# Optimization experiments

Measured on AMD Instinct MI355X. Metric: run time of the kernel, lower is better.

Reference implementation:

```python
import jax, jax.numpy as jnp
import numpy as np

EPS = 1e-5
TOPK = 4

def bn(x, gamma, beta, mean, var, axis=1):
    # inference-mode batchnorm (running stats)
    shp = [1] * x.ndim
    shp[axis] = -1
    scale = (gamma / jnp.sqrt(var + EPS)).reshape(shp)
    shift = (beta - mean * gamma / jnp.sqrt(var + EPS)).reshape(shp)
    return x * scale + shift


def setup_inputs() -> dict:
    key = jax.random.key(0)
    ks = jax.random.split(key, 4)
    B, C, T, H, W = 8, 512, 8, 28, 28
    R = 64
    Cq = C // 4
    s = 0.05
    return {
        "input": jax.random.normal(ks[0], (B, C, T, H, W), dtype=jnp.float32),
        "w_reduce": jax.random.normal(ks[1], (R, C), dtype=jnp.float32) * s,
        "bn1_gamma": jnp.ones((R,), jnp.float32), "bn1_beta": jnp.zeros((R,), jnp.float32),
        "bn1_mean": jnp.zeros((R,), jnp.float32), "bn1_var": jnp.ones((R,), jnp.float32),
        "w_proj": jax.random.normal(ks[2], (Cq, C + 2), dtype=jnp.float32) * s,
        "bn2_gamma": jnp.ones((Cq,), jnp.float32), "bn2_beta": jnp.zeros((Cq,), jnp.float32),
        "bn2_mean": jnp.zeros((Cq,), jnp.float32), "bn2_var": jnp.ones((Cq,), jnp.float32),
        "w_t": jax.random.normal(ks[3], (C, Cq, 3, 1), dtype=jnp.float32) * s,
        "bn3_gamma": jnp.ones((C,), jnp.float32), "bn3_beta": jnp.zeros((C,), jnp.float32),
        "bn3_mean": jnp.zeros((C,), jnp.float32), "bn3_var": jnp.ones((C,), jnp.float32),
    }


def reference(input, w_reduce, bn1_gamma, bn1_beta, bn1_mean, bn1_var,
              w_proj, bn2_gamma, bn2_beta, bn2_mean, bn2_var,
              w_t, bn3_gamma, bn3_beta, bn3_mean, bn3_var):
    x = input
    B, C, T, H, W = x.shape
    R = w_reduce.shape[0]
    K = TOPK
    HW = H * W

    # spatial template from frame 0
    template_d = x[:, :, 0].reshape(B, C, HW)                                  # (B,C,HW)
    template_p = bn(jnp.einsum('rc,bcs->brs', w_reduce, template_d),
                    bn1_gamma, bn1_beta, bn1_mean, bn1_var)                     # (B,R,HW)
    spt_inds = jnp.argmax(template_p, axis=2)                                  # (B,R)
    template_resample = jnp.take_along_axis(template_d, spt_inds[:, None, :], axis=2)  # (B,C,R)

    x_flat = x.reshape(B, C, T * HW)
    affinity = jnp.einsum('bcr,bcs->brs', template_resample, x_flat)           # (B,R,T*HW)
    affinity = affinity.reshape(B, R, T, HW)
    _, topk_inds = jax.lax.top_k(affinity, K)                                  # (B,R,T,K)
    inds = jnp.transpose(topk_inds, (0, 3, 2, 1))                              # (B,K,T,R)

    # gather trajectory features: traj[b,k,c,t,r] = x[b,c,t, inds[b,k,t,r]]
    x4 = x.reshape(B, C, T, HW)
    traj = jnp.take_along_axis(x4[:, None], inds[:, :, None], axis=4)          # (B,K,C,T,R)
    traj_bk = traj.reshape(B * K, C, T, R)

    inds_bk = inds.reshape(B * K, 1, T, R)
    row = (inds_bk // W).astype(jnp.float32) / H
    col = (inds_bk % W).astype(jnp.float32) / W
    coords = jnp.concatenate([row, col], axis=1)                               # (B*K,2,T,R)

    fuse = jnp.concatenate([traj_bk, coords], axis=1)                          # (B*K,C+2,T,R)
    fuse = bn(jnp.einsum('qc,bctr->bqtr', w_proj, fuse),
              bn2_gamma, bn2_beta, bn2_mean, bn2_var)                          # (B*K,C/4,T,R)
    fuse = fuse.reshape(B, K, C // 4, T, R).max(axis=1)                        # (B,C/4,T,R)

    tc = jax.lax.conv_general_dilated(fuse, w_t, window_strides=(1, 1),
                                      padding=((1, 1), (0, 0)),
                                      dimension_numbers=('NCHW', 'OIHW', 'NCHW'))
    tc = jax.nn.relu(bn(tc, bn3_gamma, bn3_beta, bn3_mean, bn3_var))           # (B,C,T,R)

    points = traj.mean(axis=1).reshape(B, C, T * R)                            # (B,C,T*R)
    proj = jnp.einsum('bcp,bcs->bps', points, x_flat)                          # (B,T*R,T*HW)
    proj = jax.nn.softmax(proj, axis=1)                                        # softmax over T*R (dim=1)
    prop = jnp.einsum('bcp,bps->bcs', tc.reshape(B, C, T * R), proj)           # (B,C,T*HW)
    return x + prop.reshape(B, C, T, H, W)
```

## Files before the change

kernel.cpp:

```cpp
#include <hip/hip_runtime.h>

#define EPSB 1e-5f

#define B_   8
#define C_   512
#define T_   8
#define HW_  784
#define S_   6272
#define R_   64
#define CQ_  128
#define K_   4
#define P_   512

typedef _Float16 f16;
typedef __attribute__((ext_vector_type(8))) _Float16 f16x8;
typedef __attribute__((ext_vector_type(4))) _Float16 f16x4;
typedef __attribute__((ext_vector_type(4))) float    f32x4;

#define OB_PTST  0ull
#define OB_TC    4194304ull
#define OB_D     8388608ull
#define OB_TRH   8589312ull
#define OB_TRF   9113600ull
#define OB_INDS  10162176ull
#define OB_WRH   10227712ull
#define OB_WPH   10293248ull
#define OB_WTH   10424320ull
#define OB_XT    10817536ull
#define T_TPA    62197760ull
#define T_AFF    63803392ull
#define T_FUSEK  62197760ull
#define T_FUSE   66392064ull
#define CHB      62197760ull

__device__ __forceinline__ void gload16(const void* g, void* l) {
    __builtin_amdgcn_global_load_lds(
        (const __attribute__((address_space(1))) unsigned int*)g,
        (__attribute__((address_space(3))) unsigned int*)l, 16, 0, 0);
}

__global__ __launch_bounds__(256) void k_prep(
    const float* __restrict__ wr, const float* __restrict__ wp,
    const float* __restrict__ wt,
    f16* __restrict__ wrh, f16* __restrict__ wph, f16* __restrict__ wth)
{
    int i = blockIdx.x*256 + threadIdx.x;
    if (i < 32768) {
        wrh[i] = (f16)wr[i];
    } else if (i < 98304) {
        int j = i - 32768;
        int q = j >> 9, c = j & 511;
        wph[j] = (f16)wp[q*514 + c];
    } else {
        int j = i - 98304;
        int co = j / 384;
        int rem = j - co*384;
        int dt = rem >> 7, ci = rem & 127;
        wth[j] = (f16)wt[(size_t)(co*CQ_ + ci)*3 + dt];
    }
}

__global__ __launch_bounds__(256) void k_xpose(
    const float* __restrict__ x, f16* __restrict__ xT)
{
    __shared__ float tile[64][65];
    int s0 = blockIdx.x*64, c0 = blockIdx.y*64, b = blockIdx.z;
    int tid = threadIdx.x;
    #pragma unroll
    for (int i = 0; i < 4; ++i) {
        int idx = tid + i*256;
        int cl = idx >> 4, s4 = (idx & 15)*4;
        f32x4 v = *(const f32x4*)&x[((size_t)(b*C_ + c0+cl))*S_ + s0 + s4];
        tile[cl][s4] = v.x; tile[cl][s4+1] = v.y;
        tile[cl][s4+2] = v.z; tile[cl][s4+3] = v.w;
    }
    __syncthreads();
    #pragma unroll
    for (int i = 0; i < 4; ++i) {
        int idx = tid + i*256;
        int sl = idx >> 4, c4 = (idx & 15)*4;
        f16x4 h;
        h[0] = (f16)tile[c4+0][sl]; h[1] = (f16)tile[c4+1][sl];
        h[2] = (f16)tile[c4+2][sl]; h[3] = (f16)tile[c4+3][sl];
        *(f16x4*)&xT[((size_t)(b*S_ + s0+sl))*C_ + c0 + c4] = h;
    }
}

__global__ __launch_bounds__(256) void k_templ(
    const f16* __restrict__ xT, const f16* __restrict__ wrh,
    float* __restrict__ tpa)
{
    __shared__ __align__(16) f16 As[128*64];
    __shared__ __align__(16) f16 Bs[64*64];
    int b = blockIdx.y; int s0 = blockIdx.x*128;
    int tid = threadIdx.x;
    int lane = tid & 63, w = tid >> 6;
    int lrow = lane >> 3;
    int swzc = ((lane & 7) ^ lrow) * 8;
    const f16* ga = xT  + ((size_t)b*S_ + s0 + w*32 + lrow)*C_ + swzc;
    const f16* gb = wrh + (size_t)(w*16 + lrow)*C_ + swzc;
    int mbase = (w & 1)*64, nbase = (w >> 1)*32;
    int fr = lane & 15, quad = lane >> 4;
    int sw = fr & 7;
    f32x4 acc[4][2] = {};
    for (int c0 = 0; c0 < C_; c0 += 64) {
        #pragma unroll
        for (int j = 0; j < 4; ++j)
            gload16(ga + j*8*C_, &As[(w*32 + j*8)*64]);
        #pragma unroll
        for (int j = 0; j < 2; ++j)
            gload16(gb + j*8*C_, &Bs[(w*16 + j*8)*64]);
        ga += 64; gb += 64;
        __syncthreads();
        #pragma unroll
        for (int kk = 0; kk < 2; ++kk) {
            int ch = ((kk*4 + quad) ^ sw) * 8;
            f16x8 af[4], bf[2];
            #pragma unroll
            for (int mt = 0; mt < 4; ++mt)
                af[mt] = *(const f16x8*)&As[(mbase + mt*16 + fr)*64 + ch];
            #pragma unroll
            for (int nt = 0; nt < 2; ++nt)
                bf[nt] = *(const f16x8*)&Bs[(nbase + nt*16 + fr)*64 + ch];
            #pragma unroll
            for (int mt = 0; mt < 4; ++mt)
                #pragma unroll
                for (int nt = 0; nt < 2; ++nt)
                    acc[mt][nt] = __builtin_amdgcn_mfma_f32_16x16x32_f16(
                        af[mt], bf[nt], acc[mt][nt], 0, 0, 0);
        }
        __syncthreads();
    }
    #pragma unroll
    for (int mt = 0; mt < 4; ++mt) {
        int sb = s0 + mbase + mt*16 + quad*4;
        if (sb < HW_) {
            #pragma unroll
            for (int nt = 0; nt < 2; ++nt) {
                int r = nbase + nt*16 + fr;
                *(f32x4*)&tpa[((size_t)(b*R_ + r))*HW_ + sb] = acc[mt][nt];
            }
        }
    }
}

__global__ __launch_bounds__(256) void k_targmax(
    const float* __restrict__ x, const float* __restrict__ wr_g,
    const float* __restrict__ g1, const float* __restrict__ v1,
    const float* __restrict__ tpa,
    float* __restrict__ trf, f16* __restrict__ trh)
{
    __shared__ float row[HW_];
    __shared__ float sval[256];
    __shared__ int   sidx[256];
    __shared__ float cval[4];
    __shared__ int   cidx[4];
    __shared__ float eval_[4];
    __shared__ int   bestind;
    int bid = blockIdx.x;
    int b = bid >> 6, r = bid & 63;
    int tid = threadIdx.x;
    float sc = g1[r] * rsqrtf(v1[r] + EPSB);
    const float* tprow = tpa + (size_t)bid*HW_;
    for (int s = tid; s < HW_; s += 256) row[s] = tprow[s]*sc;
    __syncthreads();
    for (int pass = 0; pass < 4; ++pass) {
        float best = -INFINITY; int bi = 0;
        for (int s = tid; s < HW_; s += 256) {
            float v = row[s];
            if (v > best) { best = v; bi = s; }
        }
        sval[tid] = best; sidx[tid] = bi;
        __syncthreads();
        for (int off = 128; off > 0; off >>= 1) {
            if (tid < off) {
                float ov = sval[tid+off]; int oi = sidx[tid+off];
                if (ov > sval[tid] || (ov == sval[tid] && oi < sidx[tid])) {
                    sval[tid] = ov; sidx[tid] = oi;
                }
            }
            __syncthreads();
        }
        if (tid == 0) {
            cval[pass] = sval[0]; cidx[pass] = sidx[0];
            row[sidx[0]] = -INFINITY;
        }
        __syncthreads();
    }
    float thr = 0.05f * fabsf(sc);
    if (cval[0] - cval[1] >= thr) {
        if (tid == 0) bestind = cidx[0];
    } else {
        int w = tid >> 6, lane = tid & 63;
        int cand = cidx[w];
        float sum = 0.f;
        #pragma unroll
        for (int i = 0; i < 8; ++i) {
            int c = lane + i*64;
            sum += wr_g[r*C_ + c] * x[((size_t)(b*C_ + c))*S_ + cand];
        }
        #pragma unroll
        for (int off = 32; off > 0; off >>= 1) sum += __shfl_xor(sum, off);
        if (lane == 0) eval_[w] = sum*sc;
        __syncthreads();
        if (tid == 0) {
            float bv = eval_[0]; int bi2 = cidx[0];
            for (int j = 1; j < 4; ++j) {
                float v = eval_[j]; int ii = cidx[j];
                if (v > bv || (v == bv && ii < bi2)) { bv = v; bi2 = ii; }
            }
            bestind = bi2;
        }
    }
    __syncthreads();
    int ind = bestind;
    for (int c = tid; c < C_; c += 256) {
        float v = x[((size_t)(b*C_ + c))*S_ + ind];
        trf[(size_t)bid*C_ + c] = v;
        trh[(size_t)bid*C_ + c] = (f16)v;
    }
}

__global__ __launch_bounds__(256) void k_affin(
    const f16* __restrict__ xT, const f16* __restrict__ trh,
    float* __restrict__ aff)
{
    __shared__ __align__(16) f16 As[128*64];
    __shared__ __align__(16) f16 Bs[64*64];
    int b = blockIdx.y; int s0 = blockIdx.x*128;
    int tid = threadIdx.x;
    int lane = tid & 63, w = tid >> 6;
    int lrow = lane >> 3;
    int swzc = ((lane & 7) ^ lrow) * 8;
    const f16* ga = xT  + ((size_t)b*S_ + s0 + w*32 + lrow)*C_ + swzc;
    const f16* gb = trh + ((size_t)(b*R_) + w*16 + lrow)*C_ + swzc;
    int mbase = (w & 1)*64, nbase = (w >> 1)*32;
    int fr = lane & 15, quad = lane >> 4;
    int sw = fr & 7;
    f32x4 acc[4][2] = {};
    for (int c0 = 0; c0 < C_; c0 += 64) {
        #pragma unroll
        for (int j = 0; j < 4; ++j)
            gload16(ga + j*8*C_, &As[(w*32 + j*8)*64]);
        #pragma unroll
        for (int j = 0; j < 2; ++j)
            gload16(gb + j*8*C_, &Bs[(w*16 + j*8)*64]);
        ga += 64; gb += 64;
        __syncthreads();
        #pragma unroll
        for (int kk = 0; kk < 2; ++kk) {
            int ch = ((kk*4 + quad) ^ sw) * 8;
            f16x8 af[4], bf[2];
            #pragma unroll
            for (int mt = 0; mt < 4; ++mt)
                af[mt] = *(const f16x8*)&As[(mbase + mt*16 + fr)*64 + ch];
            #pragma unroll
            for (int nt = 0; nt < 2; ++nt)
                bf[nt] = *(const f16x8*)&Bs[(nbase + nt*16 + fr)*64 + ch];
            #pragma unroll
            for (int mt = 0; mt < 4; ++mt)
                #pragma unroll
                for (int nt = 0; nt < 2; ++nt)
                    acc[mt][nt] = __builtin_amdgcn_mfma_f32_16x16x32_f16(
                        af[mt], bf[nt], acc[mt][nt], 0, 0, 0);
        }
        __syncthreads();
    }
    #pragma unroll
    for (int mt = 0; mt < 4; ++mt) {
        int sb = s0 + mbase + mt*16 + quad*4;
        #pragma unroll
        for (int nt = 0; nt < 2; ++nt) {
            int r = nbase + nt*16 + fr;
            *(f32x4*)&aff[((size_t)(b*R_ + r))*S_ + sb] = acc[mt][nt];
        }
    }
}

__global__ __launch_bounds__(256) void k_topk(
    const float* __restrict__ x, const float* __restrict__ trf,
    const float* __restrict__ aff, int* __restrict__ inds)
{
    __shared__ float row[HW_];
    __shared__ float sval[256];
    __shared__ int   sidx[256];
    __shared__ float cval[8];
    __shared__ int   cidx[8];
    __shared__ float eval_[8];
    int r = blockIdx.x, t = blockIdx.y, b = blockIdx.z;
    int tid = threadIdx.x;
    const float* arow = aff + ((size_t)(b*R_ + r))*S_ + t*HW_;
    for (int s = tid; s < HW_; s += 256) row[s] = arow[s];
    __syncthreads();
    for (int pass = 0; pass < 8; ++pass) {
        float best = -INFINITY; int bi = 0;
        for (int s = tid; s < HW_; s += 256) {
            float v = row[s];
            if (v > best) { best = v; bi = s; }
        }
        sval[tid] = best; sidx[tid] = bi;
        __syncthreads();
        for (int off = 128; off > 0; off >>= 1) {
            if (tid < off) {
                float ov = sval[tid+off]; int oi = sidx[tid+off];
                if (ov > sval[tid] || (ov == sval[tid] && oi < sidx[tid])) {
                    sval[tid] = ov; sidx[tid] = oi;
                }
            }
            __syncthreads();
        }
        if (tid == 0) {
            cval[pass] = sval[0]; cidx[pass] = sidx[0];
            row[sidx[0]] = -INFINITY;
        }
        __syncthreads();
    }
    if (cval[3] - cval[4] >= 0.35f) {
        if (tid < K_)
            inds[((b*K_ + tid)*T_ + t)*R_ + r] = cidx[tid];
    } else {
        int w = tid >> 6, lane = tid & 63;
        #pragma unroll
        for (int half = 0; half < 2; ++half) {
            int j = w + half*4;
            int cand = cidx[j];
            float sum = 0.f;
            #pragma unroll
            for (int i = 0; i < 8; ++i) {
                int c = lane + i*64;
                sum += trf[((size_t)(b*R_ + r))*C_ + c]
                     * x[((size_t)(b*C_ + c))*S_ + t*HW_ + cand];
            }
            #pragma unroll
            for (int off = 32; off > 0; off >>= 1) sum += __shfl_xor(sum, off);
            if (lane == 0) eval_[j] = sum;
        }
        __syncthreads();
        if (tid == 0) {
            unsigned used = 0;
            for (int k = 0; k < K_; ++k) {
                float bv = -INFINITY; int bj = -1;
                for (int j = 0; j < 8; ++j) {
                    if (used & (1u << j)) continue;
                    float v = eval_[j]; int ii = cidx[j];
                    if (bj < 0 || v > bv || (v == bv && ii < cidx[bj])) {
                        bv = v; bj = j;
                    }
                }
                used |= 1u << bj;
                inds[((b*K_ + k)*T_ + t)*R_ + r] = cidx[bj];
            }
        }
    }
}

__global__ __launch_bounds__(256) void k_pointsT(
    const float* __restrict__ x, const int* __restrict__ inds,
    f16* __restrict__ ptsT)
{
    __shared__ float tile[64][65];
    __shared__ int   indl[4][64];
    int c0 = blockIdx.x*64, t = blockIdx.y, b = blockIdx.z;
    int tid = threadIdx.x;
    {
        int k = tid >> 6, r = tid & 63;
        indl[k][r] = inds[((b*K_ + k)*T_ + t)*R_ + r];
    }
    __syncthreads();
    #pragma unroll
    for (int i = 0; i < 16; ++i) {
        int idx = tid + i*256;
        int cl = idx >> 6, r = idx & 63;
        const float* base = x + (size_t)(b*C_ + c0 + cl)*S_ + t*HW_;
        float v = base[indl[0][r]] + base[indl[1][r]] + base[indl[2][r]] + base[indl[3][r]];
        tile[cl][r] = 0.25f*v;
    }
    __syncthreads();
    #pragma unroll
    for (int i = 0; i < 16; ++i) {
        int idx = tid + i*256;
        int rl = idx >> 6, cl = idx & 63;
        ptsT[((size_t)b*P_ + t*64 + rl)*C_ + c0 + cl] = (f16)tile[cl][rl];
    }
}

__global__ __launch_bounds__(256) void k_fuse(
    const f16* __restrict__ xT, const f16* __restrict__ wph,
    const float* __restrict__ wp,
    const float* __restrict__ g2, const float* __restrict__ b2,
    const float* __restrict__ m2, const float* __restrict__ v2,
    f16* __restrict__ fusekT, const int* __restrict__ inds)
{
    __shared__ __align__(16) f16 As[128*32];
    __shared__ __align__(16) f16 Bs[64*32];
    __shared__ float scq[128], shq[128], wrq[128], wcq[128];
    __shared__ float rowv[64], colv[64];
    int bid = blockIdx.x;
    int t = bid & 7, bk = bid >> 3;
    int b = bk >> 2;
    int tid = threadIdx.x;
    int lane = tid & 63, w = tid >> 6;
    if (tid < 128) {
        float sc = g2[tid] * rsqrtf(v2[tid] + EPSB);
        scq[tid] = sc;
        shq[tid] = b2[tid] - m2[tid]*sc;
        wrq[tid] = wp[tid*514 + 512];
        wcq[tid] = wp[tid*514 + 513];
    } else if (tid < 192) {
        int r = tid - 128;
        int id = inds[bk*T_*R_ + t*R_ + r];
        rowv[r] = (float)(id / 28) * (1.0f/28.0f);
        colv[r] = (float)(id % 28) * (1.0f/28.0f);
    }
    int srow = w*16 + (lane >> 2);
    int scol = (lane & 3)*8;
    int ind = inds[bk*T_*R_ + t*R_ + srow];
    const f16* ga = wph + (size_t)srow*C_ + scol;
    const f16* gb = xT + ((size_t)b*S_ + t*HW_ + ind)*C_ + scol;
    int mbase = (w & 1)*64, nbase = (w >> 1)*32;
    int fr = lane & 15, fk = (lane >> 4)*8, quad = lane >> 4;
    f32x4 acc[4][2] = {};
    for (int c0 = 0; c0 < C_; c0 += 32) {
        gload16(ga,         &As[w*512]);
        gload16(ga + 64*C_, &As[2048 + w*512]);
        gload16(gb,         &Bs[w*512]);
        ga += 32; gb += 32;
        __syncthreads();
        f16x8 af[4], bf[2];
        #pragma unroll
        for (int mt = 0; mt < 4; ++mt)
            af[mt] = *(const f16x8*)&As[(mbase + mt*16 + fr)*32 + fk];
        #pragma unroll
        for (int nt = 0; nt < 2; ++nt)
            bf[nt] = *(const f16x8*)&Bs[(nbase + nt*16 + fr)*32 + fk];
        #pragma unroll
        for (int mt = 0; mt < 4; ++mt)
            #pragma unroll
            for (int nt = 0; nt < 2; ++nt)
                acc[mt][nt] = __builtin_amdgcn_mfma_f32_16x16x32_f16(
                    af[mt], bf[nt], acc[mt][nt], 0, 0, 0);
        __syncthreads();
    }
    #pragma unroll
    for (int mt = 0; mt < 4; ++mt) {
        int qb = mbase + mt*16 + quad*4;
        #pragma unroll
        for (int nt = 0; nt < 2; ++nt) {
            int r = nbase + nt*16 + fr;
            f16x4 h;
            #pragma unroll
            for (int i = 0; i < 4; ++i) {
                int q = qb + i;
                float v = acc[mt][nt][i] + wrq[q]*rowv[r] + wcq[q]*colv[r];
                h[i] = (f16)(v*scq[q] + shq[q]);
            }
            *(f16x4*)&fusekT[((size_t)bk*P_ + t*R_ + r)*CQ_ + qb] = h;
        }
    }
}

__global__ __launch_bounds__(256) void k_maxk(
    const f16* __restrict__ fusekT, f16* __restrict__ fuseT)
{
    int idx8 = (blockIdx.x*256 + threadIdx.x)*8;
    int b = idx8 >> 16;
    int pq = idx8 & 65535;
    const f16* base = fusekT + (size_t)(b*4)*65536 + pq;
    f16x8 v0 = *(const f16x8*)base;
    #pragma unroll
    for (int k = 1; k < K_; ++k) {
        f16x8 vk = *(const f16x8*)(base + (size_t)k*65536);
        #pragma unroll
        for (int j = 0; j < 8; ++j)
            v0[j] = (float)vk[j] > (float)v0[j] ? vk[j] : v0[j];
    }
    *(f16x8*)&fuseT[(size_t)b*65536 + pq] = v0;
}

__global__ __launch_bounds__(256) void k_conv(
    const f16* __restrict__ wth,
    const float* __restrict__ g3, const float* __restrict__ b3,
    const float* __restrict__ m3, const float* __restrict__ v3,
    const f16* __restrict__ fuseT, f16* __restrict__ tc)
{
    __shared__ __align__(16) f16 As[128*64];
    __shared__ __align__(16) f16 Bs[128*64];
    int p0 = blockIdx.x*128, c0 = blockIdx.y*128, b = blockIdx.z;
    int tid = threadIdx.x;
    int lane = tid & 63, w = tid >> 6;
    int lrow = lane >> 3;
    int swzc = ((lane & 7) ^ lrow) * 8;
    int mrow = (w & 1)*64, nrow = (w >> 1)*64;
    int fr = lane & 15, quad = lane >> 4;
    int sw = fr & 7;
    f32x4 acc[4][4] = {};
    for (int step = 0; step < 6; ++step) {
        int dt = step >> 1, h = step & 1;
        int shift = (dt - 1)*64;
        #pragma unroll
        for (int j = 0; j < 4; ++j) {
            int rb = w*32 + j*8;
            int pg = p0 + rb + shift;
            if (pg >= 0 && pg < P_)
                gload16(fuseT + ((size_t)b*P_ + pg + lrow)*CQ_ + h*64 + swzc,
                        &As[rb*64]);
            else
                *(f32x4*)((char*)&As[rb*64] + lane*16) = (f32x4){0.f,0.f,0.f,0.f};
        }
        #pragma unroll
        for (int j = 0; j < 4; ++j) {
            int rb = w*32 + j*8;
            gload16(wth + (size_t)(c0 + rb + lrow)*384 + dt*128 + h*64 + swzc,
                    &Bs[rb*64]);
        }
        __syncthreads();
        #pragma unroll
        for (int kk = 0; kk < 2; ++kk) {
            int ch = ((kk*4 + quad) ^ sw) * 8;
            f16x8 af[4], bf[4];
            #pragma unroll
            for (int mt = 0; mt < 4; ++mt)
                af[mt] = *(const f16x8*)&As[(mrow + mt*16 + fr)*64 + ch];
            #pragma unroll
            for (int nt = 0; nt < 4; ++nt)
                bf[nt] = *(const f16x8*)&Bs[(nrow + nt*16 + fr)*64 + ch];
            #pragma unroll
            for (int mt = 0; mt < 4; ++mt)
                #pragma unroll
                for (int nt = 0; nt < 4; ++nt)
                    acc[mt][nt] = __builtin_amdgcn_mfma_f32_16x16x32_f16(
                        af[mt], bf[nt], acc[mt][nt], 0, 0, 0);
        }
        __syncthreads();
    }
    #pragma unroll
    for (int nt = 0; nt < 4; ++nt) {
        int co = c0 + nrow + nt*16 + fr;
        float sc = g3[co] * rsqrtf(v3[co] + EPSB);
        float sh = b3[co] - m3[co]*sc;
        #pragma unroll
        for (int mt = 0; mt < 4; ++mt) {
            int p = p0 + mrow + mt*16 + quad*4;
            f16x4 hv;
            #pragma unroll
            for (int i = 0; i < 4; ++i)
                hv[i] = (f16)fmaxf(acc[mt][nt][i]*sc + sh, 0.f);
            *(f16x4*)&tc[((size_t)(b*C_ + co))*P_ + p] = hv;
        }
    }
}

__global__ __launch_bounds__(256) void k_gemmL(
    const f16* __restrict__ xT, const f16* __restrict__ ptsT,
    float* __restrict__ LT, int st, int NCHb)
{
    __shared__ __align__(16) f16 As[128*64];
    __shared__ __align__(16) f16 Bs[128*64];
    int lt = blockIdx.x; int b = blockIdx.z;
    int s0 = (st + lt)*128, p0 = blockIdx.y*128;
    int tid = threadIdx.x;
    int lane = tid & 63, w = tid >> 6;
    int lrow = lane >> 3;
    int swzc = ((lane & 7) ^ lrow) * 8;
    const f16* ga = xT   + ((size_t)b*S_ + s0 + w*32 + lrow)*C_ + swzc;
    const f16* gb = ptsT + ((size_t)b*P_ + p0 + w*32 + lrow)*C_ + swzc;
    float* Lg = LT + ((size_t)(b*NCHb + lt))*128*P_;
    int mrow = (w & 1)*64, nrow = (w >> 1)*64;
    int fr = lane & 15, quad = lane >> 4;
    int sw = fr & 7;
    f32x4 acc[4][4] = {};
    for (int c0 = 0; c0 < C_; c0 += 64) {
        #pragma unroll
        for (int j = 0; j < 4; ++j)
            gload16(ga + j*8*C_, &As[(w*32 + j*8)*64]);
        #pragma unroll
        for (int j = 0; j < 4; ++j)
            gload16(gb + j*8*C_, &Bs[(w*32 + j*8)*64]);
        ga += 64; gb += 64;
        __syncthreads();
        #pragma unroll
        for (int kk = 0; kk < 2; ++kk) {
            int ch = ((kk*4 + quad) ^ sw) * 8;
            f16x8 af[4], bf[4];
            #pragma unroll
            for (int mt = 0; mt < 4; ++mt)
                af[mt] = *(const f16x8*)&As[(mrow + mt*16 + fr)*64 + ch];
            #pragma unroll
            for (int nt = 0; nt < 4; ++nt)
                bf[nt] = *(const f16x8*)&Bs[(nrow + nt*16 + fr)*64 + ch];
            #pragma unroll
            for (int nt = 0; nt < 4; ++nt)
                #pragma unroll
                for (int mt = 0; mt < 4; ++mt)
                    acc[nt][mt] = __builtin_amdgcn_mfma_f32_16x16x32_f16(
                        bf[nt], af[mt], acc[nt][mt], 0, 0, 0);
        }
        __syncthreads();
    }
    #pragma unroll
    for (int mt = 0; mt < 4; ++mt) {
        int srow_l = mrow + mt*16 + fr;
        #pragma unroll
        for (int nt = 0; nt < 4; ++nt) {
            int p = p0 + nrow + nt*16 + quad*4;
            *(f32x4*)&Lg[(size_t)srow_l*P_ + p] = acc[nt][mt];
        }
    }
}

__global__ __launch_bounds__(256) void k_softmaxW(
    const float* __restrict__ LT, f16* __restrict__ W,
    float* __restrict__ Dinv, int st, int NCHb)
{
    int b = blockIdx.y;
    int tid = threadIdx.x, w = tid >> 6, lane = tid & 63;
    int gr = blockIdx.x*4 + w;
    int lt = gr >> 7, lrow = gr & 127;
    size_t base = ((size_t)(b*NCHb + lt)*128 + lrow)*P_;
    const float* row = LT + base + lane*8;
    f32x4 v0 = *(const f32x4*)row;
    f32x4 v1 = *(const f32x4*)(row + 4);
    float m = fmaxf(fmaxf(fmaxf(v0.x, v0.y), fmaxf(v0.z, v0.w)),
                    fmaxf(fmaxf(v1.x, v1.y), fmaxf(v1.z, v1.w)));
    #pragma unroll
    for (int off = 1; off < 64; off <<= 1) m = fmaxf(m, __shfl_xor(m, off));
    float e[8];
    e[0] = __expf(v0.x - m); e[1] = __expf(v0.y - m);
    e[2] = __expf(v0.z - m); e[3] = __expf(v0.w - m);
    e[4] = __expf(v1.x - m); e[5] = __expf(v1.y - m);
    e[6] = __expf(v1.z - m); e[7] = __expf(v1.w - m);
    float sum = ((e[0]+e[1])+(e[2]+e[3])) + ((e[4]+e[5])+(e[6]+e[7]));
    #pragma unroll
    for (int off = 1; off < 64; off <<= 1) sum += __shfl_xor(sum, off);
    f16x8 h;
    #pragma unroll
    for (int j = 0; j < 8; ++j) h[j] = (f16)e[j];
    *(f16x8*)&W[base + lane*8] = h;
    if (lane == 0) Dinv[(size_t)b*S_ + (st + lt)*128 + lrow] = 1.0f/sum;
}

__global__ __launch_bounds__(256) void k_gemmP(
    const f16* __restrict__ tc, const f16* __restrict__ W,
    const float* __restrict__ Dinv, const float* __restrict__ x,
    float* __restrict__ out, int st, int NCHb)
{
    __shared__ __align__(16) f16 As[128*64];
    __shared__ __align__(16) f16 Bs[128*64];
    int lt = blockIdx.x; int b = blockIdx.z;
    int s0 = (st + lt)*128, c0t = blockIdx.y*128;
    int tid = threadIdx.x;
    int lane = tid & 63, w = tid >> 6;
    int lrow = lane >> 3;
    int swzc = ((lane & 7) ^ lrow) * 8;
    const f16* ga = tc + ((size_t)(b*C_) + c0t + w*32 + lrow)*P_ + swzc;
    const f16* gb = W  + ((size_t)(b*NCHb + lt)*128 + w*32 + lrow)*P_ + swzc;
    int mrow = (w & 1)*64, nrow = (w >> 1)*64;
    int fr = lane & 15, quad = lane >> 4;
    int sw = fr & 7;
    f32x4 acc[4][4] = {};
    for (int p0 = 0; p0 < P_; p0 += 64) {
        #pragma unroll
        for (int j = 0; j < 4; ++j)
            gload16(ga + j*8*P_, &As[(w*32 + j*8)*64]);
        #pragma unroll
        for (int j = 0; j < 4; ++j)
            gload16(gb + j*8*P_, &Bs[(w*32 + j*8)*64]);
        ga += 64; gb += 64;
        __syncthreads();
        #pragma unroll
        for (int kk = 0; kk < 2; ++kk) {
            int ch = ((kk*4 + quad) ^ sw) * 8;
            f16x8 af[4], bf[4];
            #pragma unroll
            for (int mt = 0; mt < 4; ++mt)
                af[mt] = *(const f16x8*)&As[(mrow + mt*16 + fr)*64 + ch];
            #pragma unroll
            for (int nt = 0; nt < 4; ++nt)
                bf[nt] = *(const f16x8*)&Bs[(nrow + nt*16 + fr)*64 + ch];
            #pragma unroll
            for (int nt = 0; nt < 4; ++nt)
                #pragma unroll
                for (int mt = 0; mt < 4; ++mt)
                    acc[nt][mt] = __builtin_amdgcn_mfma_f32_16x16x32_f16(
                        bf[nt], af[mt], acc[nt][mt], 0, 0, 0);
        }
        __syncthreads();
    }
    #pragma unroll
    for (int nt = 0; nt < 4; ++nt) {
        int s = s0 + nrow + nt*16 + quad*4;
        f32x4 dv = *(const f32x4*)&Dinv[(size_t)b*S_ + s];
        #pragma unroll
        for (int mt = 0; mt < 4; ++mt) {
            int c = c0t + mrow + mt*16 + fr;
            size_t o = ((size_t)(b*C_ + c))*S_ + s;
            f32x4 xv = *(const f32x4*)&x[o];
            f32x4 res = xv + acc[nt][mt]*dv;
            *(f32x4*)&out[o] = res;
        }
    }
}

extern "C" void kernel_launch(void* const* d_in, const int* in_sizes, int n_in,
                              void* d_out, int out_size, void* d_ws, size_t ws_size,
                              hipStream_t stream) {
    const float* x   = (const float*)d_in[0];
    const float* wrd = (const float*)d_in[1];
    const float* g1  = (const float*)d_in[2];
    const float* v1  = (const float*)d_in[5];
    const float* wp  = (const float*)d_in[6];
    const float* g2  = (const float*)d_in[7];
    const float* b2  = (const float*)d_in[8];
    const float* m2  = (const float*)d_in[9];
    const float* v2  = (const float*)d_in[10];
    const float* wt  = (const float*)d_in[11];
    const float* g3  = (const float*)d_in[12];
    const float* b3  = (const float*)d_in[13];
    const float* m3  = (const float*)d_in[14];
    const float* v3  = (const float*)d_in[15];
    char*  wsb = (char*)d_ws;
    float* out = (float*)d_out;

    f16*   ptsT  = (f16*)  (wsb + OB_PTST);
    f16*   tc    = (f16*)  (wsb + OB_TC);
    float* Dinv  = (float*)(wsb + OB_D);
    f16*   trh   = (f16*)  (wsb + OB_TRH);
    float* trf   = (float*)(wsb + OB_TRF);
    int*   inds  = (int*)  (wsb + OB_INDS);
    f16*   wrh   = (f16*)  (wsb + OB_WRH);
    f16*   wph   = (f16*)  (wsb + OB_WPH);
    f16*   wth   = (f16*)  (wsb + OB_WTH);
    f16*   xT    = (f16*)  (wsb + OB_XT);
    float* tpa   = (float*)(wsb + T_TPA);
    float* aff   = (float*)(wsb + T_AFF);
    f16*   fusekT= (f16*)  (wsb + T_FUSEK);
    f16*   fuseT = (f16*)  (wsb + T_FUSE);

    const size_t PER_TILE = 3145728ull;
    size_t avail = ws_size > CHB ? ws_size - CHB : 0;
    int NCH = (int)(avail / PER_TILE);
    if (NCH < 1) NCH = 1;
    if (NCH > 49) NCH = 49;
    int nchunks = (49 + NCH - 1)/NCH;
    int NCHb = (49 + nchunks - 1)/nchunks;
    float* LT = (float*)(wsb + CHB);
    f16*   W  = (f16*)  (wsb + CHB + (size_t)NCHb*8ull*128ull*P_*4ull);

    k_prep<<<1152, 256, 0, stream>>>(wrd, wp, wt, wrh, wph, wth);
    k_xpose<<<dim3(98, 8, 8), 256, 0, stream>>>(x, xT);
    k_templ<<<dim3(7, 8), 256, 0, stream>>>(xT, wrh, tpa);
    k_targmax<<<512, 256, 0, stream>>>(x, wrd, g1, v1, tpa, trf, trh);
    k_affin<<<dim3(49, 8), 256, 0, stream>>>(xT, trh, aff);
    k_topk<<<dim3(R_, T_, B_), 256, 0, stream>>>(x, trf, aff, inds);
    k_pointsT<<<dim3(8, 8, 8), 256, 0, stream>>>(x, inds, ptsT);
    k_fuse<<<256, 256, 0, stream>>>(xT, wph, wp, g2, b2, m2, v2, fusekT, inds);
    k_maxk<<<256, 256, 0, stream>>>(fusekT, fuseT);
    k_conv<<<dim3(4, 4, 8), 256, 0, stream>>>(wth, g3, b3, m3, v3, fuseT, tc);

    for (int st = 0; st < 49; st += NCHb) {
        int cnt = (49 - st) < NCHb ? (49 - st) : NCHb;
        k_gemmL<<<dim3(cnt, 4, 8), 256, 0, stream>>>(xT, ptsT, LT, st, NCHb);
        k_softmaxW<<<dim3(cnt*32, 8), 256, 0, stream>>>(LT, W, Dinv, st, NCHb);
        k_gemmP<<<dim3(cnt, 4, 8), 256, 0, stream>>>(tc, W, Dinv, x, out, st, NCHb);
    }
}
```

Baseline: 519.8 us.

## Fuse logits GEMM with softmax and double-buffer affinity and propagation GEMMs

Merges k_gemmL and k_softmaxW into one 512-thread kernel. Each block computes a full 128x512 logit tile in registers, reduces row max and sum across waves through shared memory, and writes the f16 exponentials and inverse sums directly. This drops the fp32 logit round-trip through global memory, which also lets each chunk tile shrink so more chunks fit per pass. Separately, k_affin and k_gemmP get double-buffered shared-memory staging so the next K-slice loads while MFMAs run. In exchange, register pressure rises (32 accumulators per thread), the fused kernel launches only 49x8 blocks, and shared-memory use grows.

```diff
diff --git a/kernel.cpp b/kernel.cpp
--- a/kernel.cpp
+++ b/kernel.cpp
@@ -225,8 +225,8 @@
     const f16* __restrict__ xT, const f16* __restrict__ trh,
     float* __restrict__ aff)
 {
-    __shared__ __align__(16) f16 As[128*64];
-    __shared__ __align__(16) f16 Bs[64*64];
+    __shared__ __align__(16) f16 As[2][128*64];
+    __shared__ __align__(16) f16 Bs[2][64*64];
     int b = blockIdx.y; int s0 = blockIdx.x*128;
     int tid = threadIdx.x;
     int lane = tid & 63, w = tid >> 6;
@@ -238,25 +238,35 @@
     int fr = lane & 15, quad = lane >> 4;
     int sw = fr & 7;
     f32x4 acc[4][2] = {};
+    #pragma unroll
+    for (int j = 0; j < 4; ++j)
+        gload16(ga + j*8*C_, &As[0][(w*32 + j*8)*64]);
+    #pragma unroll
+    for (int j = 0; j < 2; ++j)
+        gload16(gb + j*8*C_, &Bs[0][(w*16 + j*8)*64]);
+    ga += 64; gb += 64;
+    __syncthreads();
+    int cur = 0;
     for (int c0 = 0; c0 < C_; c0 += 64) {
-        #pragma unroll
-        for (int j = 0; j < 4; ++j)
-            gload16(ga + j*8*C_, &As[(w*32 + j*8)*64]);
-        #pragma unroll
-        for (int j = 0; j < 2; ++j)
-            gload16(gb + j*8*C_, &Bs[(w*16 + j*8)*64]);
-        ga += 64; gb += 64;
-        __syncthreads();
+        if (c0 + 64 < C_) {
+            #pragma unroll
+            for (int j = 0; j < 4; ++j)
+                gload16(ga + j*8*C_, &As[cur^1][(w*32 + j*8)*64]);
+            #pragma unroll
+            for (int j = 0; j < 2; ++j)
+                gload16(gb + j*8*C_, &Bs[cur^1][(w*16 + j*8)*64]);
+            ga += 64; gb += 64;
+        }
         #pragma unroll
         for (int kk = 0; kk < 2; ++kk) {
             int ch = ((kk*4 + quad) ^ sw) * 8;
             f16x8 af[4], bf[2];
             #pragma unroll
             for (int mt = 0; mt < 4; ++mt)
-                af[mt] = *(const f16x8*)&As[(mbase + mt*16 + fr)*64 + ch];
+                af[mt] = *(const f16x8*)&As[cur][(mbase + mt*16 + fr)*64 + ch];
             #pragma unroll
             for (int nt = 0; nt < 2; ++nt)
-                bf[nt] = *(const f16x8*)&Bs[(nbase + nt*16 + fr)*64 + ch];
+                bf[nt] = *(const f16x8*)&Bs[cur][(nbase + nt*16 + fr)*64 + ch];
             #pragma unroll
             for (int mt = 0; mt < 4; ++mt)
                 #pragma unroll
@@ -265,6 +275,7 @@
                         af[mt], bf[nt], acc[mt][nt], 0, 0, 0);
         }
         __syncthreads();
+        cur ^= 1;
     }
     #pragma unroll
     for (int mt = 0; mt < 4; ++mt) {
@@ -550,46 +561,46 @@
     }
 }
 
-__global__ __launch_bounds__(256) void k_gemmL(
+__global__ __launch_bounds__(512, 2) void k_attnW(
     const f16* __restrict__ xT, const f16* __restrict__ ptsT,
-    float* __restrict__ LT, int st, int NCHb)
+    f16* __restrict__ W, float* __restrict__ Dinv, int st, int NCHb)
 {
     __shared__ __align__(16) f16 As[128*64];
-    __shared__ __align__(16) f16 Bs[128*64];
+    __shared__ __align__(16) f16 Bs[512*64];
+    __shared__ float red[128][4];
     int lt = blockIdx.x; int b = blockIdx.z;
-    int s0 = (st + lt)*128, p0 = blockIdx.y*128;
+    int s0 = (st + lt)*128;
     int tid = threadIdx.x;
     int lane = tid & 63, w = tid >> 6;
+    int wr = w & 1, wc = w >> 1;
     int lrow = lane >> 3;
     int swzc = ((lane & 7) ^ lrow) * 8;
-    const f16* ga = xT   + ((size_t)b*S_ + s0 + w*32 + lrow)*C_ + swzc;
-    const f16* gb = ptsT + ((size_t)b*P_ + p0 + w*32 + lrow)*C_ + swzc;
-    float* Lg = LT + ((size_t)(b*NCHb + lt))*128*P_;
-    int mrow = (w & 1)*64, nrow = (w >> 1)*64;
+    const f16* ga = xT   + ((size_t)b*S_ + s0 + w*16 + lrow)*C_ + swzc;
+    const f16* gb = ptsT + ((size_t)b*P_ + w*64 + lrow)*C_ + swzc;
     int fr = lane & 15, quad = lane >> 4;
     int sw = fr & 7;
-    f32x4 acc[4][4] = {};
+    f32x4 acc[8][4] = {};
     for (int c0 = 0; c0 < C_; c0 += 64) {
         #pragma unroll
-        for (int j = 0; j < 4; ++j)
-            gload16(ga + j*8*C_, &As[(w*32 + j*8)*64]);
-        #pragma unroll
-        for (int j = 0; j < 4; ++j)
-            gload16(gb + j*8*C_, &Bs[(w*32 + j*8)*64]);
+        for (int j = 0; j < 2; ++j)
+            gload16(ga + j*8*C_, &As[(w*16 + j*8)*64]);
+        #pragma unroll
+        for (int j = 0; j < 8; ++j)
+            gload16(gb + j*8*C_, &Bs[(w*64 + j*8)*64]);
         ga += 64; gb += 64;
         __syncthreads();
         #pragma unroll
         for (int kk = 0; kk < 2; ++kk) {
             int ch = ((kk*4 + quad) ^ sw) * 8;
-            f16x8 af[4], bf[4];
+            f16x8 af[4], bf[8];
             #pragma unroll
             for (int mt = 0; mt < 4; ++mt)
-                af[mt] = *(const f16x8*)&As[(mrow + mt*16 + fr)*64 + ch];
-            #pragma unroll
-            for (int nt = 0; nt < 4; ++nt)
-                bf[nt] = *(const f16x8*)&Bs[(nrow + nt*16 + fr)*64 + ch];
-            #pragma unroll
-            for (int nt = 0; nt < 4; ++nt)
+                af[mt] = *(const f16x8*)&As[(wr*64 + mt*16 + fr)*64 + ch];
+            #pragma unroll
+            for (int nt = 0; nt < 8; ++nt)
+                bf[nt] = *(const f16x8*)&Bs[(wc*128 + nt*16 + fr)*64 + ch];
+            #pragma unroll
+            for (int nt = 0; nt < 8; ++nt)
                 #pragma unroll
                 for (int mt = 0; mt < 4; ++mt)
                     acc[nt][mt] = __builtin_amdgcn_mfma_f32_16x16x32_f16(
@@ -597,46 +608,58 @@
         }
         __syncthreads();
     }
+    float M[4];
     #pragma unroll
     for (int mt = 0; mt < 4; ++mt) {
-        int srow_l = mrow + mt*16 + fr;
-        #pragma unroll
-        for (int nt = 0; nt < 4; ++nt) {
-            int p = p0 + nrow + nt*16 + quad*4;
-            *(f32x4*)&Lg[(size_t)srow_l*P_ + p] = acc[nt][mt];
-        }
-    }
-}
-
-__global__ __launch_bounds__(256) void k_softmaxW(
-    const float* __restrict__ LT, f16* __restrict__ W,
-    float* __restrict__ Dinv, int st, int NCHb)
-{
-    int b = blockIdx.y;
-    int tid = threadIdx.x, w = tid >> 6, lane = tid & 63;
-    int gr = blockIdx.x*4 + w;
-    int lt = gr >> 7, lrow = gr & 127;
-    size_t base = ((size_t)(b*NCHb + lt)*128 + lrow)*P_;
-    const float* row = LT + base + lane*8;
-    f32x4 v0 = *(const f32x4*)row;
-    f32x4 v1 = *(const f32x4*)(row + 4);
-    float m = fmaxf(fmaxf(fmaxf(v0.x, v0.y), fmaxf(v0.z, v0.w)),
-                    fmaxf(fmaxf(v1.x, v1.y), fmaxf(v1.z, v1.w)));
-    #pragma unroll
-    for (int off = 1; off < 64; off <<= 1) m = fmaxf(m, __shfl_xor(m, off));
-    float e[8];
-    e[0] = __expf(v0.x - m); e[1] = __expf(v0.y - m);
-    e[2] = __expf(v0.z - m); e[3] = __expf(v0.w - m);
-    e[4] = __expf(v1.x - m); e[5] = __expf(v1.y - m);
-    e[6] = __expf(v1.z - m); e[7] = __expf(v1.w - m);
-    float sum = ((e[0]+e[1])+(e[2]+e[3])) + ((e[4]+e[5])+(e[6]+e[7]));
-    #pragma unroll
-    for (int off = 1; off < 64; off <<= 1) sum += __shfl_xor(sum, off);
-    f16x8 h;
-    #pragma unroll
-    for (int j = 0; j < 8; ++j) h[j] = (f16)e[j];
-    *(f16x8*)&W[base + lane*8] = h;
-    if (lane == 0) Dinv[(size_t)b*S_ + (st + lt)*128 + lrow] = 1.0f/sum;
+        float m = -INFINITY;
+        #pragma unroll
+        for (int nt = 0; nt < 8; ++nt)
+            #pragma unroll
+            for (int i = 0; i < 4; ++i)
+                m = fmaxf(m, acc[nt][mt][i]);
+        m = fmaxf(m, __shfl_xor(m, 16));
+        m = fmaxf(m, __shfl_xor(m, 32));
+        if (quad == 0) red[wr*64 + mt*16 + fr][wc] = m;
+    }
+    __syncthreads();
+    #pragma unroll
+    for (int mt = 0; mt < 4; ++mt) {
+        int srow = wr*64 + mt*16 + fr;
+        M[mt] = fmaxf(fmaxf(red[srow][0], red[srow][1]),
+                      fmaxf(red[srow][2], red[srow][3]));
+    }
+    __syncthreads();
+    #pragma unroll
+    for (int mt = 0; mt < 4; ++mt) {
+        float s = 0.f;
+        #pragma unroll
+        for (int nt = 0; nt < 8; ++nt)
+            #pragma unroll
+            for (int i = 0; i < 4; ++i) {
+                float e = __expf(acc[nt][mt][i] - M[mt]);
+                acc[nt][mt][i] = e;
+                s += e;
+            }
+        s += __shfl_xor(s, 16);
+        s += __shfl_xor(s, 32);
+        if (quad == 0) red[wr*64 + mt*16 + fr][wc] = s;
+    }
+    __syncthreads();
+    size_t wbase = (size_t)(b*NCHb + lt)*128*(size_t)P_;
+    #pragma unroll
+    for (int mt = 0; mt < 4; ++mt) {
+        int srow = wr*64 + mt*16 + fr;
+        float tot = (red[srow][0] + red[srow][1]) + (red[srow][2] + red[srow][3]);
+        if (wc == 0 && quad == 0)
+            Dinv[(size_t)b*S_ + s0 + srow] = 1.0f/tot;
+        #pragma unroll
+        for (int nt = 0; nt < 8; ++nt) {
+            f16x4 h;
+            #pragma unroll
+            for (int i = 0; i < 4; ++i) h[i] = (f16)acc[nt][mt][i];
+            *(f16x4*)&W[wbase + (size_t)srow*P_ + wc*128 + nt*16 + quad*4] = h;
+        }
+    }
 }
 
 __global__ __launch_bounds__(256) void k_gemmP(
@@ -644,8 +667,8 @@
     const float* __restrict__ Dinv, const float* __restrict__ x,
     float* __restrict__ out, int st, int NCHb)
 {
-    __shared__ __align__(16) f16 As[128*64];
-    __shared__ __align__(16) f16 Bs[128*64];
+    __shared__ __align__(16) f16 As[2][128*64];
+    __shared__ __align__(16) f16 Bs[2][128*64];
     int lt = blockIdx.x; int b = blockIdx.z;
     int s0 = (st + lt)*128, c0t = blockIdx.y*128;
     int tid = threadIdx.x;
@@ -658,25 +681,35 @@
     int fr = lane & 15, quad = lane >> 4;
     int sw = fr & 7;
     f32x4 acc[4][4] = {};
+    #pragma unroll
+    for (int j = 0; j < 4; ++j)
+        gload16(ga + j*8*P_, &As[0][(w*32 + j*8)*64]);
+    #pragma unroll
+    for (int j = 0; j < 4; ++j)
+        gload16(gb + j*8*P_, &Bs[0][(w*32 + j*8)*64]);
+    ga += 64; gb += 64;
+    __syncthreads();
+    int cur = 0;
     for (int p0 = 0; p0 < P_; p0 += 64) {
-        #pragma unroll
-        for (int j = 0; j < 4; ++j)
-            gload16(ga + j*8*P_, &As[(w*32 + j*8)*64]);
-        #pragma unroll
-        for (int j = 0; j < 4; ++j)
-            gload16(gb + j*8*P_, &Bs[(w*32 + j*8)*64]);
-        ga += 64; gb += 64;
-        __syncthreads();
+        if (p0 + 64 < P_) {
+            #pragma unroll
+            for (int j = 0; j < 4; ++j)
+                gload16(ga + j*8*P_, &As[cur^1][(w*32 + j*8)*64]);
+            #pragma unroll
+            for (int j = 0; j < 4; ++j)
+                gload16(gb + j*8*P_, &Bs[cur^1][(w*32 + j*8)*64]);
+            ga += 64; gb += 64;
+        }
         #pragma unroll
         for (int kk = 0; kk < 2; ++kk) {
             int ch = ((kk*4 + quad) ^ sw) * 8;
             f16x8 af[4], bf[4];
             #pragma unroll
             for (int mt = 0; mt < 4; ++mt)
-                af[mt] = *(const f16x8*)&As[(mrow + mt*16 + fr)*64 + ch];
+                af[mt] = *(const f16x8*)&As[cur][(mrow + mt*16 + fr)*64 + ch];
             #pragma unroll
             for (int nt = 0; nt < 4; ++nt)
-                bf[nt] = *(const f16x8*)&Bs[(nrow + nt*16 + fr)*64 + ch];
+                bf[nt] = *(const f16x8*)&Bs[cur][(nrow + nt*16 + fr)*64 + ch];
             #pragma unroll
             for (int nt = 0; nt < 4; ++nt)
                 #pragma unroll
@@ -685,6 +718,7 @@
                         bf[nt], af[mt], acc[nt][mt], 0, 0, 0);
         }
         __syncthreads();
+        cur ^= 1;
     }
     #pragma unroll
     for (int nt = 0; nt < 4; ++nt) {
@@ -736,15 +770,14 @@
     f16*   fusekT= (f16*)  (wsb + T_FUSEK);
     f16*   fuseT = (f16*)  (wsb + T_FUSE);
 
-    const size_t PER_TILE = 3145728ull;
+    const size_t PER_TILE = 1048576ull;
     size_t avail = ws_size > CHB ? ws_size - CHB : 0;
     int NCH = (int)(avail / PER_TILE);
     if (NCH < 1) NCH = 1;
     if (NCH > 49) NCH = 49;
     int nchunks = (49 + NCH - 1)/NCH;
     int NCHb = (49 + nchunks - 1)/nchunks;
-    float* LT = (float*)(wsb + CHB);
-    f16*   W  = (f16*)  (wsb + CHB + (size_t)NCHb*8ull*128ull*P_*4ull);
+    f16* W = (f16*)(wsb + CHB);
 
     k_prep<<<1152, 256, 0, stream>>>(wrd, wp, wt, wrh, wph, wth);
     k_xpose<<<dim3(98, 8, 8), 256, 0, stream>>>(x, xT);
@@ -759,8 +792,7 @@
 
     for (int st = 0; st < 49; st += NCHb) {
         int cnt = (49 - st) < NCHb ? (49 - st) : NCHb;
-        k_gemmL<<<dim3(cnt, 4, 8), 256, 0, stream>>>(xT, ptsT, LT, st, NCHb);
-        k_softmaxW<<<dim3(cnt*32, 8), 256, 0, stream>>>(LT, W, Dinv, st, NCHb);
+        k_attnW<<<dim3(cnt, 1, 8), 512, 0, stream>>>(xT, ptsT, W, Dinv, st, NCHb);
         k_gemmP<<<dim3(cnt, 4, 8), 256, 0, stream>>>(tc, W, Dinv, x, out, st, NCHb);
     }
 }
```

Result: faster. 484.5 us (-6.8%).
